# Kernel optimization log

Measured on AMD Instinct MI355X. Metric: run time of the kernel, lower is better.

The kernel has to match this reference:

```python
import jax, jax.numpy as jnp
import numpy as np

NUM_HEADS = 16
HEAD_SIZE = 64
CTXT_LEN = 2048
N_EMBED = 1024
BATCH = 2


def setup_inputs() -> dict:
    key = jax.random.key(0)
    ks = jax.random.split(key, 5)
    s = 0.02  # realistic init scale for weights
    return {
        "x": jax.random.normal(ks[0], (BATCH, CTXT_LEN, N_EMBED), dtype=jnp.float32),
        "Wk": jax.random.normal(ks[1], (N_EMBED, NUM_HEADS * HEAD_SIZE), dtype=jnp.float32) * s,
        "bk": jnp.zeros((NUM_HEADS * HEAD_SIZE,), dtype=jnp.float32),
        "Wq": jax.random.normal(ks[2], (N_EMBED, NUM_HEADS * HEAD_SIZE), dtype=jnp.float32) * s,
        "bq": jnp.zeros((NUM_HEADS * HEAD_SIZE,), dtype=jnp.float32),
        "Wv": jax.random.normal(ks[3], (N_EMBED, NUM_HEADS * HEAD_SIZE), dtype=jnp.float32) * s,
        "bv": jnp.zeros((NUM_HEADS * HEAD_SIZE,), dtype=jnp.float32),
        "Wo": jax.random.normal(ks[4], (NUM_HEADS * HEAD_SIZE, N_EMBED), dtype=jnp.float32) * s,
        "bo": jnp.zeros((N_EMBED,), dtype=jnp.float32),
    }


def reference(x, Wk, bk, Wq, bq, Wv, bv, Wo, bo):
    B, T, E = x.shape
    H, D = NUM_HEADS, HEAD_SIZE
    # QKV projections -> [B, T, H, D]
    k = (x @ Wk + bk).reshape(B, T, H, D)
    q = (x @ Wq + bq).reshape(B, T, H, D)
    v = (x @ Wv + bv).reshape(B, T, H, D)
    # NOTE: source scales by 1/sqrt(n_embed), not 1/sqrt(head_size)
    scale = 1.0 / (E ** 0.5)
    wei = jnp.einsum('bthd,bshd->bhts', q, k) * scale  # [B, H, T, T]
    causal = jnp.tril(jnp.ones((T, T), dtype=bool))
    wei = jnp.where(causal, wei, -jnp.inf)
    wei = jax.nn.softmax(wei, axis=-1)
    # dropout p=0.0 -> identity
    out = jnp.einsum('bhts,bshd->bthd', wei, v).reshape(B, T, H * D)
    return out @ Wo + bo
```

## Files before the change

### kernel.cpp

```cpp
#include <hip/hip_runtime.h>

#define NH 16
#define HS 64
#define T_CTX 2048
#define NE 1024
#define NB 2
#define BT (NB*T_CTX)
#define HD (NH*HS)

typedef unsigned short u16;
typedef __bf16 bf16_t;
typedef bf16_t bf16x8 __attribute__((ext_vector_type(8)));
typedef float f32x4 __attribute__((ext_vector_type(4)));
typedef u16 u16x8 __attribute__((ext_vector_type(8)));
typedef u16 u16x4 __attribute__((ext_vector_type(4)));

#define GLDS(gp, lp) __builtin_amdgcn_global_load_lds( \
    (const __attribute__((address_space(1))) void*)(gp), \
    (__attribute__((address_space(3))) void*)(lp), 16, 0, 0)

__device__ __forceinline__ u16 f2bf(float f) {
  union { float f; unsigned u; } x; x.f = f;
  return (u16)((x.u + 0x7fffu + ((x.u >> 16) & 1u)) >> 16);
}
__device__ __forceinline__ float bf2f(u16 u) {
  union { unsigned u; float f; } x; x.u = ((unsigned)u) << 16;
  return x.f;
}
__device__ __forceinline__ unsigned pack_bf2(float hi, float lo) {
  union { float f; unsigned u; } H, L; H.f = hi; L.f = lo;
  return __builtin_amdgcn_perm(H.u + 0x8000u, L.u + 0x8000u, 0x07060302);
}

__global__ __launch_bounds__(256) void k_prep_x(const float* __restrict__ x,
                                                u16* __restrict__ xb) {
  int i = blockIdx.x * blockDim.x + threadIdx.x;
  float4 v = ((const float4*)x)[i];
  ushort4 o;
  o.x = f2bf(v.x); o.y = f2bf(v.y); o.z = f2bf(v.z); o.w = f2bf(v.w);
  ((ushort4*)xb)[i] = o;
}

__global__ __launch_bounds__(256) void k_prep_w(
    const float* __restrict__ W0, const float* __restrict__ W1,
    const float* __restrict__ W2, const float* __restrict__ W3,
    u16* __restrict__ T0, u16* __restrict__ T1,
    u16* __restrict__ T2, u16* __restrict__ T3) {
  const float* W; u16* T;
  switch (blockIdx.z) {
    case 0: W = W0; T = T0; break;
    case 1: W = W1; T = T1; break;
    case 2: W = W2; T = T2; break;
    default: W = W3; T = T3; break;
  }
  __shared__ u16 tile[64 * 72];
  int k0 = blockIdx.x * 64, n0 = blockIdx.y * 64;
  int tid = threadIdx.x;
#pragma unroll
  for (int it = 0; it < 4; ++it) {
    int ci = tid + it * 256;
    int k = ci >> 4, c = ci & 15;
    float4 v = *(const float4*)&W[(size_t)(k0 + k) * NE + n0 + c * 4];
    int n = c * 4;
    tile[(n + 0) * 72 + k] = f2bf(v.x);
    tile[(n + 1) * 72 + k] = f2bf(v.y);
    tile[(n + 2) * 72 + k] = f2bf(v.z);
    tile[(n + 3) * 72 + k] = f2bf(v.w);
  }
  __syncthreads();
#pragma unroll
  for (int it = 0; it < 2; ++it) {
    int co = tid + it * 256;
    int n = co >> 3, c = co & 7;
    u16x8 v = *(const u16x8*)&tile[n * 72 + c * 8];
    *(u16x8*)&T[(size_t)(n0 + n) * NE + k0 + c * 8] = v;
  }
}

__global__ __launch_bounds__(256) void k_gemm_qkv(
    const u16* __restrict__ xb, const u16* __restrict__ Wt,
    const float* __restrict__ bq, const float* __restrict__ bk,
    const float* __restrict__ bv, u16* __restrict__ Qw,
    u16* __restrict__ Kw, u16* __restrict__ Vtw) {
  __shared__ u16 sh[3 * 8192];
  const int z = blockIdx.z;
  const u16* W = Wt + (size_t)z * NE * HD;
  const float* bias = (z == 0) ? bq : (z == 1 ? bk : bv);
  const float scale = (z == 0) ? 0.03125f * 1.4426950408889634f : 1.0f;
  const int m0 = blockIdx.y * 128, n0 = blockIdx.x * 128;
  const int tid = threadIdx.x;
  const int lane = tid & 63, w = tid >> 6;
  const int wm = (w >> 1) * 64, wn = (w & 1) * 64, q = lane >> 4, l16 = lane & 15;

  auto stage = [&](int k0, int b) {
    u16* As = sh + b * 8192;
    u16* Bs = As + 4096;
#pragma unroll
    for (int s2 = 0; s2 < 2; ++s2) {
      int ci = w * 64 + lane + s2 * 256;
      int row = ci >> 2, cc = ci & 3;
      GLDS(xb + (size_t)(m0 + row) * NE + k0 + cc * 8, As + (size_t)(w * 64 + s2 * 256) * 8);
      GLDS(W  + (size_t)(n0 + row) * NE + k0 + cc * 8, Bs + (size_t)(w * 64 + s2 * 256) * 8);
    }
  };

  f32x4 acc[4][4];
#pragma unroll
  for (int i = 0; i < 4; ++i)
#pragma unroll
    for (int j = 0; j < 4; ++j)
#pragma unroll
      for (int r = 0; r < 4; ++r) acc[i][j][r] = 0.f;

  stage(0, 0);
  stage(32, 1);
  for (int kt = 0; kt < 32; ++kt) {
    u16* As = sh + (kt % 3) * 8192;
    u16* Bs = As + 4096;
    if (kt + 1 < 32)
      asm volatile("s_waitcnt vmcnt(4)\n\ts_barrier" ::: "memory");
    else
      asm volatile("s_waitcnt vmcnt(0)\n\ts_barrier" ::: "memory");
    if (kt + 2 < 32) stage((kt + 2) * 32, (kt + 2) % 3);
    bf16x8 av[4], bv4[4];
#pragma unroll
    for (int i = 0; i < 4; ++i) av[i]  = *(const bf16x8*)&As[(wm + i * 16 + l16) * 32 + q * 8];
#pragma unroll
    for (int j = 0; j < 4; ++j) bv4[j] = *(const bf16x8*)&Bs[(wn + j * 16 + l16) * 32 + q * 8];
#pragma unroll
    for (int i = 0; i < 4; ++i)
#pragma unroll
      for (int j = 0; j < 4; ++j)
        acc[i][j] = __builtin_amdgcn_mfma_f32_16x16x32_bf16(av[i], bv4[j], acc[i][j], 0, 0, 0);
  }
  __syncthreads();
  u16* Es = sh;

  const int bb = m0 >> 11;
  if (z == 2) {
#pragma unroll
    for (int j = 0; j < 4; ++j) {
      int n = wn + j * 16 + l16;
      float bn = bias[n0 + n];
#pragma unroll
      for (int i = 0; i < 4; ++i) {
        int m = wm + i * 16 + q * 4;
        u16x4 pk;
#pragma unroll
        for (int r = 0; r < 4; ++r) pk[r] = f2bf(acc[i][j][r] + bn);
        *(u16x4*)&Es[n * 132 + m] = pk;
      }
    }
    __syncthreads();
#pragma unroll
    for (int it = 0; it < 8; ++it) {
      int idx = it * 256 + tid;
      int dl = idx >> 4, c = idx & 15;
      u16x8 v = *(const u16x8*)&Es[dl * 132 + c * 8];
      int ng = n0 + dl, h = ng >> 6, d = ng & 63;
      int tt = (m0 & (T_CTX - 1)) + c * 8;
      *(u16x8*)&Vtw[((size_t)((bb * NH + h) * HS + d)) * T_CTX + tt] = v;
    }
  } else {
    u16* dst = (z == 0) ? Qw : Kw;
#pragma unroll
    for (int j = 0; j < 4; ++j) {
      int n = wn + j * 16 + l16;
      float bn = bias[n0 + n];
#pragma unroll
      for (int i = 0; i < 4; ++i)
#pragma unroll
        for (int r = 0; r < 4; ++r) {
          int m = wm + i * 16 + q * 4 + r;
          Es[m * 132 + n] = f2bf((acc[i][j][r] + bn) * scale);
        }
    }
    __syncthreads();
#pragma unroll
    for (int it = 0; it < 8; ++it) {
      int idx = it * 256 + tid;
      int tl = idx >> 4, c = idx & 15;
      u16x8 v = *(const u16x8*)&Es[tl * 132 + c * 8];
      int ng = n0 + c * 8, h = ng >> 6, d = ng & 63;
      int tt = (m0 & (T_CTX - 1)) + tl;
      *(u16x8*)&dst[(((size_t)(bb * NH + h)) * T_CTX + tt) * HS + d] = v;
    }
  }
}

__device__ __forceinline__ void stage_kv(const u16* __restrict__ Kp,
                                         const u16* __restrict__ Vp,
                                         int k0, u16* KsB, u16* VsB, int tid) {
#pragma unroll
  for (int it = 0; it < 2; ++it) {
    int ci = tid + it * 256;
    int row = ci >> 3, cc = ci & 7;
    int prow = (row & 32) | ((row & 12) << 1) | ((row & 16) >> 2) | (row & 3);
    int sw = (cc ^ (row & 7)) * 8;
    GLDS(Kp + (size_t)(k0 + prow) * HS + sw, KsB + ci * 8);
    GLDS(Vp + (size_t)row * T_CTX + k0 + sw, VsB + ci * 8);
  }
}

__global__ __launch_bounds__(256) void k_attn(
    const u16* __restrict__ Qw, const u16* __restrict__ Kw,
    const u16* __restrict__ Vtw, u16* __restrict__ op0,
    u16* __restrict__ op1, u16* __restrict__ op2,
    float* __restrict__ lsum) {
  __shared__ u16 Ks[3 * 64 * 64];
  __shared__ u16 Vs[3 * 64 * 64];

  const int bh = blockIdx.y;
  const int x = blockIdx.x;
  const int qt = 15 - x / 3;
  const int part = x - (15 - qt) * 3;
  const int ntiles = 2 * (qt + 1);
  const int npt = (ntiles + 2) / 3;
  const int klo = part * npt;
  const int khi = min(klo + npt, ntiles);
  const int qbase = qt * 128;

  const u16* Qp = Qw + (size_t)bh * T_CTX * HS;
  const u16* Kp = Kw + (size_t)bh * T_CTX * HS;
  const u16* Vp = Vtw + (size_t)bh * HS * T_CTX;

  const int tid = threadIdx.x, lane = tid & 63, w = tid >> 6;
  const int q = lane >> 4, c = lane & 15;
  const int rbase = w * 32;

  bf16x8 aq[2][2];
#pragma unroll
  for (int i = 0; i < 2; ++i)
#pragma unroll
    for (int s = 0; s < 2; ++s)
      aq[i][s] = *(const bf16x8*)&Qp[(size_t)(qbase + rbase + i * 16 + c) * HS + s * 32 + q * 8];

  f32x4 o[2][4];
  float lrow[2] = {0.f, 0.f};
#pragma unroll
  for (int i = 0; i < 2; ++i)
#pragma unroll
    for (int j = 0; j < 4; ++j)
#pragma unroll
      for (int r = 0; r < 4; ++r) o[i][j][r] = 0.f;

  if (klo < khi)     stage_kv(Kp, Vp, klo * 64,       Ks,        Vs,        tid);
  if (klo + 1 < khi) stage_kv(Kp, Vp, (klo + 1) * 64, Ks + 4096, Vs + 4096, tid);

  for (int kt = klo; kt < khi; ++kt) {
    const int k0 = kt * 64;
    const int idx = kt - klo;
    u16* KsB = Ks + (idx % 3) * 4096;
    u16* VsB = Vs + (idx % 3) * 4096;
    if (kt + 1 < khi) {
      asm volatile("s_waitcnt vmcnt(4)\n\ts_barrier" ::: "memory");
    } else {
      asm volatile("s_waitcnt vmcnt(0)\n\ts_barrier" ::: "memory");
    }
    if (kt + 2 < khi)
      stage_kv(Kp, Vp, (kt + 2) * 64,
               Ks + ((idx + 2) % 3) * 4096, Vs + ((idx + 2) % 3) * 4096, tid);

    f32x4 s[4][2];
#pragma unroll
    for (int i2 = 0; i2 < 4; ++i2) {
      int krow = i2 * 16 + c;
      bf16x8 kf0 = *(const bf16x8*)&KsB[krow * 64 + ((0 + q) ^ (krow & 7)) * 8];
      bf16x8 kf1 = *(const bf16x8*)&KsB[krow * 64 + ((4 + q) ^ (krow & 7)) * 8];
#pragma unroll
      for (int j2 = 0; j2 < 2; ++j2) {
        f32x4 z4 = {0.f, 0.f, 0.f, 0.f};
        z4 = __builtin_amdgcn_mfma_f32_16x16x32_bf16(kf0, aq[j2][0], z4, 0, 0, 0);
        s[i2][j2] = __builtin_amdgcn_mfma_f32_16x16x32_bf16(kf1, aq[j2][1], z4, 0, 0, 0);
      }
    }

    if (k0 + 63 > qbase + rbase) {
#pragma unroll
      for (int i2 = 0; i2 < 4; ++i2)
#pragma unroll
        for (int j2 = 0; j2 < 2; ++j2)
#pragma unroll
          for (int r = 0; r < 4; ++r) {
            int key = k0 + ((i2 >> 1) << 5) + (q << 3) + ((i2 & 1) << 2) + r;
            int qrow = qbase + rbase + j2 * 16 + c;
            if (key > qrow) s[i2][j2][r] = -1e30f;
          }
    }

#pragma unroll
    for (int i2 = 0; i2 < 4; ++i2)
#pragma unroll
      for (int j2 = 0; j2 < 2; ++j2)
#pragma unroll
        for (int r = 0; r < 4; ++r) {
          float p = __builtin_amdgcn_exp2f(s[i2][j2][r]);
          s[i2][j2][r] = p;
          lrow[j2] += p;
        }

#pragma unroll
    for (int ks = 0; ks < 2; ++ks) {
      bf16x8 bv4[4];
#pragma unroll
      for (int j = 0; j < 4; ++j) {
        int d = j * 16 + c;
        bv4[j] = *(const bf16x8*)&VsB[d * 64 + ((ks * 4 + q) ^ (d & 7)) * 8];
      }
#pragma unroll
      for (int i = 0; i < 2; ++i) {
        union { uint4 u; bf16x8 b; } af;
        af.u.x = pack_bf2(s[2 * ks][i][1],     s[2 * ks][i][0]);
        af.u.y = pack_bf2(s[2 * ks][i][3],     s[2 * ks][i][2]);
        af.u.z = pack_bf2(s[2 * ks + 1][i][1], s[2 * ks + 1][i][0]);
        af.u.w = pack_bf2(s[2 * ks + 1][i][3], s[2 * ks + 1][i][2]);
#pragma unroll
        for (int j = 0; j < 4; ++j)
          o[i][j] = __builtin_amdgcn_mfma_f32_16x16x32_bf16(af.b, bv4[j], o[i][j], 0, 0, 0);
      }
    }
  }

  u16* op = (part == 0) ? op0 : (part == 1 ? op1 : op2);
  const size_t row0 = (size_t)bh * T_CTX + qbase;
#pragma unroll
  for (int i = 0; i < 2; ++i) {
    lrow[i] += __shfl_xor(lrow[i], 16, 64);
    lrow[i] += __shfl_xor(lrow[i], 32, 64);
  }
  if (q == 0) {
#pragma unroll
    for (int i = 0; i < 2; ++i)
      lsum[(size_t)part * 65536 + row0 + rbase + i * 16 + c] = lrow[i];
  }
#pragma unroll
  for (int i = 0; i < 2; ++i)
#pragma unroll
    for (int r = 0; r < 4; ++r) {
      size_t t = row0 + rbase + i * 16 + q * 4 + r;
#pragma unroll
      for (int j = 0; j < 4; ++j)
        op[t * 64 + j * 16 + c] = f2bf(o[i][j][r]);
    }
}

__global__ __launch_bounds__(256) void k_combine(
    const u16* __restrict__ op0, const u16* __restrict__ op1,
    const u16* __restrict__ op2, const float* __restrict__ lsum,
    u16* __restrict__ att) {
  int idx = blockIdx.x * 256 + threadIdx.x;
  int row = idx >> 3, oct = idx & 7;
  float l0 = lsum[row], l1 = lsum[65536 + row], l2 = lsum[131072 + row];
  float inv = 1.f / (l0 + l1 + l2);
  u16x8 a = *(const u16x8*)&op0[(size_t)row * 64 + oct * 8];
  u16x8 b = *(const u16x8*)&op1[(size_t)row * 64 + oct * 8];
  u16x8 d = *(const u16x8*)&op2[(size_t)row * 64 + oct * 8];
  u16x8 ov;
#pragma unroll
  for (int e = 0; e < 8; ++e)
    ov[e] = f2bf((bf2f(a[e]) + bf2f(b[e]) + bf2f(d[e])) * inv);
  int bh = row >> 11, t = row & 2047, bb = bh >> 4, h = bh & 15;
  *(u16x8*)&att[((size_t)(bb * T_CTX + t)) * HD + h * 64 + oct * 8] = ov;
}

__global__ __launch_bounds__(256) void k_gemm_out(
    const u16* __restrict__ attb, const u16* __restrict__ Wot,
    const float* __restrict__ bo, float* __restrict__ out) {
  __shared__ u16 sh[3 * 6144];
  const int m0 = blockIdx.y * 64, n0 = blockIdx.x * 128;
  const int tid = threadIdx.x, lane = tid & 63, w = tid >> 6;
  const int wm = (w & 1) * 32, wn = (w >> 1) * 64;
  const int q = lane >> 4, l16 = lane & 15;

  auto stage = [&](int k0, int b) {
    u16* As = sh + b * 6144;
    u16* Bs = As + 2048;
    {
      int row = tid >> 2, cc = tid & 3;
      GLDS(attb + (size_t)(m0 + row) * NE + k0 + cc * 8, As + (size_t)tid * 8);
    }
#pragma unroll
    for (int s2 = 0; s2 < 2; ++s2) {
      int ci = tid + s2 * 256;
      int row = ci >> 2, cc = ci & 3;
      GLDS(Wot + (size_t)(n0 + row) * NE + k0 + cc * 8, Bs + (size_t)ci * 8);
    }
  };

  f32x4 acc[2][4];
#pragma unroll
  for (int i = 0; i < 2; ++i)
#pragma unroll
    for (int j = 0; j < 4; ++j)
#pragma unroll
      for (int r = 0; r < 4; ++r) acc[i][j][r] = 0.f;

  stage(0, 0);
  stage(32, 1);
  for (int kt = 0; kt < 32; ++kt) {
    u16* As = sh + (kt % 3) * 6144;
    u16* Bs = As + 2048;
    if (kt + 1 < 32)
      asm volatile("s_waitcnt vmcnt(3)\n\ts_barrier" ::: "memory");
    else
      asm volatile("s_waitcnt vmcnt(0)\n\ts_barrier" ::: "memory");
    if (kt + 2 < 32) stage((kt + 2) * 32, (kt + 2) % 3);
    bf16x8 av[2], bv4[4];
#pragma unroll
    for (int i = 0; i < 2; ++i) av[i]  = *(const bf16x8*)&As[(wm + i * 16 + l16) * 32 + q * 8];
#pragma unroll
    for (int j = 0; j < 4; ++j) bv4[j] = *(const bf16x8*)&Bs[(wn + j * 16 + l16) * 32 + q * 8];
#pragma unroll
    for (int i = 0; i < 2; ++i)
#pragma unroll
      for (int j = 0; j < 4; ++j)
        acc[i][j] = __builtin_amdgcn_mfma_f32_16x16x32_bf16(av[i], bv4[j], acc[i][j], 0, 0, 0);
  }
#pragma unroll
  for (int j = 0; j < 4; ++j) {
    int n = n0 + wn + j * 16 + l16;
    float bn = bo[n];
#pragma unroll
    for (int i = 0; i < 2; ++i)
#pragma unroll
      for (int r = 0; r < 4; ++r) {
        int m = m0 + wm + i * 16 + q * 4 + r;
        out[(size_t)m * NE + n] = acc[i][j][r] + bn;
      }
  }
}

extern "C" void kernel_launch(void* const* d_in, const int* in_sizes, int n_in,
                              void* d_out, int out_size, void* d_ws, size_t ws_size,
                              hipStream_t stream) {
  (void)in_sizes; (void)n_in; (void)out_size; (void)ws_size;
  const float* x  = (const float*)d_in[0];
  const float* Wk = (const float*)d_in[1];
  const float* bk = (const float*)d_in[2];
  const float* Wq = (const float*)d_in[3];
  const float* bq = (const float*)d_in[4];
  const float* Wv = (const float*)d_in[5];
  const float* bv = (const float*)d_in[6];
  const float* Wo = (const float*)d_in[7];
  const float* bo = (const float*)d_in[8];
  float* out = (float*)d_out;

  u16* base = (u16*)d_ws;
  const size_t M = 1024 * 1024;
  u16* xb   = base;
  u16* Wt   = base + 4 * M;
  u16* Wot  = base + 7 * M;
  u16* Qw   = base + 8 * M;
  u16* Kw   = base + 12 * M;
  u16* Vtw  = base + 16 * M;
  u16* op0  = base + 20 * M;
  u16* op1  = base + 24 * M;
  u16* op2  = base;
  float* lsum = (float*)(base + 4 * M);
  u16* attw = base + 12 * M;

  k_prep_x<<<dim3(BT * NE / 4 / 256), 256, 0, stream>>>(x, xb);
  k_prep_w<<<dim3(16, 16, 4), 256, 0, stream>>>(
      Wq, Wk, Wv, Wo, Wt, Wt + (size_t)NE * HD, Wt + (size_t)2 * NE * HD, Wot);
  k_gemm_qkv<<<dim3(8, 32, 3), 256, 0, stream>>>(xb, Wt, bq, bk, bv, Qw, Kw, Vtw);
  k_attn<<<dim3(48, 32), 256, 0, stream>>>(Qw, Kw, Vtw, op0, op1, op2, lsum);
  k_combine<<<dim3(2048), 256, 0, stream>>>(op0, op1, op2, lsum, attw);
  k_gemm_out<<<dim3(8, 64), 256, 0, stream>>>(attw, Wot, bo, out);
}
```

Measured before the change: 201.8 us.

## Swizzle GEMM LDS tiles and remap block indices for XCD locality

Adds an XOR swizzle on the 16-byte chunk index for the A/B tiles in both projection GEMMs, applied both when staging via global_load_lds and when reading fragments, to cut LDS bank conflicts. Also flattens the grids of the QKV GEMM, attention and output GEMM and remaps block ids so that blocks sharing weight columns or a head land on the same XCD (round-robin by bx&7), aiming for better L2 reuse. The tradeoff is extra index arithmetic, plus a remapping that relies on the hardware dispatching blocks round-robin across eight XCDs.

Result: faster. 184.8 us (-8.4%).

```diff
diff --git a/kernel.cpp b/kernel.cpp
--- a/kernel.cpp
+++ b/kernel.cpp
@@ -87,10 +87,14 @@
   const u16* W = Wt + (size_t)z * NE * HD;
   const float* bias = (z == 0) ? bq : (z == 1 ? bk : bv);
   const float scale = (z == 0) ? 0.03125f * 1.4426950408889634f : 1.0f;
-  const int m0 = blockIdx.y * 128, n0 = blockIdx.x * 128;
+  const int bx = blockIdx.x;
+  const int xcd = bx & 7, ii = bx >> 3;
+  const int m0 = (xcd + 8 * (ii & 3)) * 128;
+  const int n0 = (ii >> 2) * 128;
   const int tid = threadIdx.x;
   const int lane = tid & 63, w = tid >> 6;
   const int wm = (w >> 1) * 64, wn = (w & 1) * 64, q = lane >> 4, l16 = lane & 15;
+  const int qsw = q ^ ((l16 >> 1) & 3);
 
   auto stage = [&](int k0, int b) {
     u16* As = sh + b * 8192;
@@ -99,8 +103,9 @@
     for (int s2 = 0; s2 < 2; ++s2) {
       int ci = w * 64 + lane + s2 * 256;
       int row = ci >> 2, cc = ci & 3;
-      GLDS(xb + (size_t)(m0 + row) * NE + k0 + cc * 8, As + (size_t)(w * 64 + s2 * 256) * 8);
-      GLDS(W  + (size_t)(n0 + row) * NE + k0 + cc * 8, Bs + (size_t)(w * 64 + s2 * 256) * 8);
+      int cs = cc ^ ((row >> 1) & 3);
+      GLDS(xb + (size_t)(m0 + row) * NE + k0 + cs * 8, As + (size_t)ci * 8);
+      GLDS(W  + (size_t)(n0 + row) * NE + k0 + cs * 8, Bs + (size_t)ci * 8);
     }
   };
 
@@ -124,9 +129,9 @@
     if (kt + 2 < 32) stage((kt + 2) * 32, (kt + 2) % 3);
     bf16x8 av[4], bv4[4];
 #pragma unroll
-    for (int i = 0; i < 4; ++i) av[i]  = *(const bf16x8*)&As[(wm + i * 16 + l16) * 32 + q * 8];
-#pragma unroll
-    for (int j = 0; j < 4; ++j) bv4[j] = *(const bf16x8*)&Bs[(wn + j * 16 + l16) * 32 + q * 8];
+    for (int i = 0; i < 4; ++i) av[i]  = *(const bf16x8*)&As[(wm + i * 16 + l16) * 32 + qsw * 8];
+#pragma unroll
+    for (int j = 0; j < 4; ++j) bv4[j] = *(const bf16x8*)&Bs[(wn + j * 16 + l16) * 32 + qsw * 8];
 #pragma unroll
     for (int i = 0; i < 4; ++i)
 #pragma unroll
@@ -210,8 +215,10 @@
   __shared__ u16 Ks[3 * 64 * 64];
   __shared__ u16 Vs[3 * 64 * 64];
 
-  const int bh = blockIdx.y;
-  const int x = blockIdx.x;
+  const int b = blockIdx.x;
+  const int xcd = b & 7, ii = b >> 3;
+  const int bh = xcd + 8 * (ii & 3);
+  const int x = ii >> 2;
   const int qt = 15 - x / 3;
   const int part = x - (15 - qt) * 3;
   const int ntiles = 2 * (qt + 1);
@@ -367,23 +374,29 @@
     const u16* __restrict__ attb, const u16* __restrict__ Wot,
     const float* __restrict__ bo, float* __restrict__ out) {
   __shared__ u16 sh[3 * 6144];
-  const int m0 = blockIdx.y * 64, n0 = blockIdx.x * 128;
+  const int bx = blockIdx.x;
+  const int xcd = bx & 7, ii = bx >> 3;
+  const int m0 = (xcd + 8 * (ii & 7)) * 64;
+  const int n0 = (ii >> 3) * 128;
   const int tid = threadIdx.x, lane = tid & 63, w = tid >> 6;
   const int wm = (w & 1) * 32, wn = (w >> 1) * 64;
   const int q = lane >> 4, l16 = lane & 15;
+  const int qsw = q ^ ((l16 >> 1) & 3);
 
   auto stage = [&](int k0, int b) {
     u16* As = sh + b * 6144;
     u16* Bs = As + 2048;
     {
       int row = tid >> 2, cc = tid & 3;
-      GLDS(attb + (size_t)(m0 + row) * NE + k0 + cc * 8, As + (size_t)tid * 8);
+      int cs = cc ^ ((row >> 1) & 3);
+      GLDS(attb + (size_t)(m0 + row) * NE + k0 + cs * 8, As + (size_t)tid * 8);
     }
 #pragma unroll
     for (int s2 = 0; s2 < 2; ++s2) {
       int ci = tid + s2 * 256;
       int row = ci >> 2, cc = ci & 3;
-      GLDS(Wot + (size_t)(n0 + row) * NE + k0 + cc * 8, Bs + (size_t)ci * 8);
+      int cs = cc ^ ((row >> 1) & 3);
+      GLDS(Wot + (size_t)(n0 + row) * NE + k0 + cs * 8, Bs + (size_t)ci * 8);
     }
   };
 
@@ -407,9 +420,9 @@
     if (kt + 2 < 32) stage((kt + 2) * 32, (kt + 2) % 3);
     bf16x8 av[2], bv4[4];
 #pragma unroll
-    for (int i = 0; i < 2; ++i) av[i]  = *(const bf16x8*)&As[(wm + i * 16 + l16) * 32 + q * 8];
-#pragma unroll
-    for (int j = 0; j < 4; ++j) bv4[j] = *(const bf16x8*)&Bs[(wn + j * 16 + l16) * 32 + q * 8];
+    for (int i = 0; i < 2; ++i) av[i]  = *(const bf16x8*)&As[(wm + i * 16 + l16) * 32 + qsw * 8];
+#pragma unroll
+    for (int j = 0; j < 4; ++j) bv4[j] = *(const bf16x8*)&Bs[(wn + j * 16 + l16) * 32 + qsw * 8];
 #pragma unroll
     for (int i = 0; i < 2; ++i)
 #pragma unroll
@@ -462,8 +475,8 @@
   k_prep_x<<<dim3(BT * NE / 4 / 256), 256, 0, stream>>>(x, xb);
   k_prep_w<<<dim3(16, 16, 4), 256, 0, stream>>>(
       Wq, Wk, Wv, Wo, Wt, Wt + (size_t)NE * HD, Wt + (size_t)2 * NE * HD, Wot);
-  k_gemm_qkv<<<dim3(8, 32, 3), 256, 0, stream>>>(xb, Wt, bq, bk, bv, Qw, Kw, Vtw);
-  k_attn<<<dim3(48, 32), 256, 0, stream>>>(Qw, Kw, Vtw, op0, op1, op2, lsum);
+  k_gemm_qkv<<<dim3(256, 1, 3), 256, 0, stream>>>(xb, Wt, bq, bk, bv, Qw, Kw, Vtw);
+  k_attn<<<dim3(1536), 256, 0, stream>>>(Qw, Kw, Vtw, op0, op1, op2, lsum);
   k_combine<<<dim3(2048), 256, 0, stream>>>(op0, op1, op2, lsum, attw);
-  k_gemm_out<<<dim3(8, 64), 256, 0, stream>>>(attw, Wot, bo, out);
-}
+  k_gemm_out<<<dim3(512), 256, 0, stream>>>(attw, Wot, bo, out);
+}
```
